# Kernel tuning notes

Measured on AMD Instinct MI355X. Metric: run time of the kernel, lower is better.

Reference implementation:

```python
import jax, jax.numpy as jnp
import numpy as np

B, LATENT, HID, OUT, E = 8192, 128, 400, 4096, 16

def setup_inputs() -> dict:
    key = jax.random.key(0)
    k = jax.random.split(key, 6)
    return {
        "z": jax.random.normal(k[0], (B, LATENT), dtype=jnp.float32),
        "W1": jax.random.normal(k[1], (E, HID, LATENT), dtype=jnp.float32) * (1.0 / np.sqrt(LATENT)),
        "b1": jax.random.normal(k[2], (E, HID), dtype=jnp.float32) * 0.01,
        "W2": jax.random.normal(k[3], (E, OUT, HID), dtype=jnp.float32) * (1.0 / np.sqrt(HID)),
        "b2": jax.random.normal(k[4], (E, OUT), dtype=jnp.float32) * 0.01,
        "angle_idx": jax.random.randint(k[5], (B,), 0, E, dtype=jnp.int64) if jax.config.jax_enable_x64 else jax.random.randint(k[5], (B,), 0, E, dtype=jnp.int32),
    }

def reference(z, W1, b1, W2, b2, angle_idx):
    # Per-sample expert select: out[i] = sigmoid(W2[e] @ relu(W1[e] @ z[i] + b1[e]) + b2[e]), e = angle_idx[i].
    # Dense-dispatch reference: run every expert on the full batch, select per-sample result.
    n_experts = W1.shape[0]
    out = jnp.zeros((z.shape[0], W2.shape[1]), dtype=z.dtype)
    for e in range(n_experts):  # small fixed loop over experts
        h = jax.nn.relu(z @ W1[e].T + b1[e])          # [B, 400]
        o = jax.nn.sigmoid(h @ W2[e].T + b2[e])       # [B, OUT]
        out = jnp.where((angle_idx == e)[:, None], o, out)
    return out
```

## Files before the change

### kernel.cpp

```cpp
#include <hip/hip_runtime.h>

#define BATCH  8192
#define LATENT 128
#define HID    400
#define HIDP   448
#define NOUT   4096
#define NE     16
#define HROWS  (BATCH + 256)

typedef __attribute__((ext_vector_type(8))) short bf16x8;
typedef __attribute__((ext_vector_type(4))) float f32x4;

__device__ __forceinline__ unsigned short f2bf(float f){
  unsigned u = __builtin_bit_cast(unsigned, f);
  u += 0x7fffu + ((u >> 16) & 1u);
  return (unsigned short)(u >> 16);
}

__device__ __forceinline__ void gload16(const void* g, void* l){
  __builtin_amdgcn_global_load_lds(
      (const __attribute__((address_space(1))) void*)g,
      (__attribute__((address_space(3))) void*)l, 16, 0, 0);
}

__global__ __launch_bounds__(1024) void k_prep(
    const int* __restrict__ aidx, int* __restrict__ wsI,
    const float* __restrict__ W2, unsigned short* __restrict__ W2b)
{
  int tid = threadIdx.x;
  if (blockIdx.x != 0){
    const int NSLOT = NE*NOUT*(HIDP/8);
    int g = ((int)blockIdx.x - 1)*1024 + tid;
    for (int i = g; i < NSLOT; i += 1536*1024){
      int row  = (int)((unsigned)i / 56u);
      int slot = i - row*56;
      int k = slot*8;
      bf16x8 w = (bf16x8){0,0,0,0,0,0,0,0};
      if (slot < 50){
        const float* s = W2 + (size_t)row*HID + k;
        f32x4 a = __builtin_nontemporal_load((const f32x4*)s);
        f32x4 b = __builtin_nontemporal_load((const f32x4*)(s+4));
        w[0]=(short)f2bf(a.x); w[1]=(short)f2bf(a.y); w[2]=(short)f2bf(a.z); w[3]=(short)f2bf(a.w);
        w[4]=(short)f2bf(b.x); w[5]=(short)f2bf(b.y); w[6]=(short)f2bf(b.z); w[7]=(short)f2bf(b.w);
      }
      __builtin_nontemporal_store(w, (bf16x8*)(W2b + (size_t)row*HIDP + k));
    }
    return;
  }
  __shared__ int hist[NE];
  __shared__ int cursor[NE];
  int lane = tid & 63;
  if (tid < NE) hist[tid] = 0;
  __syncthreads();

  int ev[8];
  #pragma unroll
  for (int c=0;c<8;c++) ev[c] = aidx[c*1024 + tid];

  #pragma unroll
  for (int c=0;c<8;c++){
    for (int x=0;x<NE;x++){
      unsigned long long m = __ballot(ev[c]==x);
      if (lane==0 && m) atomicAdd(&hist[x], (int)__popcll(m));
    }
  }
  __syncthreads();
  if (tid==0){
    int a=0;
    for (int x=0;x<NE;x++){ cursor[x]=a; wsI[32+x]=a; a+=hist[x]; }
    wsI[32+NE]=a;
  }
  __syncthreads();

  #pragma unroll
  for (int c=0;c<8;c++){
    int e = ev[c], i = c*1024 + tid;
    for (int x=0;x<NE;x++){
      unsigned long long m = __ballot(e==x);
      if (m){
        int leader = __ffsll((unsigned long long)m) - 1;
        int base = 0;
        if (lane == leader) base = atomicAdd(&cursor[x], (int)__popcll(m));
        base = __shfl(base, leader);
        if (e==x){
          int rank = (int)__popcll(m & ((1ull<<lane)-1ull));
          wsI[64 + base + rank] = i;
        }
      }
    }
  }
}

__global__ __launch_bounds__(256) void k_layer1(
    const float* __restrict__ z, const float* __restrict__ W1, const float* __restrict__ b1,
    const int* __restrict__ wsI, unsigned short* __restrict__ hws)
{
  __shared__ int s_off[NE+1];
  __shared__ int s_perm[64];
  __shared__ unsigned short As[64*128];
  __shared__ unsigned short Bs[64*128];
  int tid = threadIdx.x;
  if (tid <= NE) s_off[tid] = wsI[32+tid];
  __syncthreads();

  int e=-1, tile=0;
  { int acc=0;
    for (int i=0;i<NE;i++){
      int cnt = s_off[i+1]-s_off[i]; int t = (cnt+63)>>6;
      if ((int)blockIdx.x < acc+t){ e=i; tile=(int)blockIdx.x-acc; break; }
      acc += t; } }
  if (e < 0) return;
  int r0 = s_off[e] + tile*64;
  int rows = s_off[e+1] - r0; if (rows > 64) rows = 64;
  int n0 = blockIdx.y * 64;

  if (tid < 64) s_perm[tid] = (tid < rows) ? wsI[64 + r0 + tid] : 0;
  __syncthreads();

  #pragma unroll
  for (int p=0;p<8;p++){
    int id = tid + p*256; int row = id>>5, c4 = id&31;
    float4 v = make_float4(0.f,0.f,0.f,0.f);
    if (row < rows) v = *(const float4*)(z + (size_t)s_perm[row]*LATENT + c4*4);
    short4 w; w.x=(short)f2bf(v.x); w.y=(short)f2bf(v.y); w.z=(short)f2bf(v.z); w.w=(short)f2bf(v.w);
    *(short4*)((char*)As + row*256 + ((c4*8) ^ ((row&7)<<4))) = w;
  }
  const float* w1e = W1 + (size_t)e*HID*LATENT;
  #pragma unroll
  for (int p=0;p<8;p++){
    int id = tid + p*256; int row = id>>5, c4 = id&31;
    int n = n0 + row;
    float4 v = make_float4(0.f,0.f,0.f,0.f);
    if (n < HID) v = *(const float4*)(w1e + (size_t)n*LATENT + c4*4);
    short4 w; w.x=(short)f2bf(v.x); w.y=(short)f2bf(v.y); w.z=(short)f2bf(v.z); w.w=(short)f2bf(v.w);
    *(short4*)((char*)Bs + row*256 + ((c4*8) ^ ((row&7)<<4))) = w;
  }
  __syncthreads();

  int lane = tid & 63, wid = tid >> 6;
  int wm = wid >> 1, wn = wid & 1;
  int llo = lane & 15, lhi = lane >> 4;
  f32x4 acc[2][2];
  #pragma unroll
  for (int i=0;i<2;i++)
    #pragma unroll
    for (int j=0;j<2;j++) acc[i][j] = (f32x4){0.f,0.f,0.f,0.f};

  #pragma unroll
  for (int s=0;s<4;s++){
    bf16x8 af[2], bfr[2];
    #pragma unroll
    for (int i=0;i<2;i++){ int m = wm*32 + i*16 + llo;
      af[i] = *(bf16x8*)((char*)As + m*256 + ((s*64 + lhi*16) ^ ((m&7)<<4))); }
    #pragma unroll
    for (int j=0;j<2;j++){ int n = wn*32 + j*16 + llo;
      bfr[j] = *(bf16x8*)((char*)Bs + n*256 + ((s*64 + lhi*16) ^ ((n&7)<<4))); }
    #pragma unroll
    for (int i=0;i<2;i++)
      #pragma unroll
      for (int j=0;j<2;j++)
        acc[i][j] = __builtin_amdgcn_mfma_f32_16x16x32_bf16(af[i], bfr[j], acc[i][j], 0,0,0);
  }

  const float* b1e = b1 + e*HID;
  #pragma unroll
  for (int i=0;i<2;i++){
    #pragma unroll
    for (int j=0;j<2;j++){
      int n = n0 + wn*32 + j*16 + llo;
      float bias = (n < HID) ? b1e[n] : 0.f;
      #pragma unroll
      for (int q=0;q<4;q++){
        int m = wm*32 + i*16 + lhi*4 + q;
        if (m < rows){
          float v = acc[i][j][q] + bias;
          v = (v > 0.f) ? v : 0.f;
          if (n >= HID) v = 0.f;
          hws[(size_t)(r0+m)*HIDP + n] = f2bf(v);
        }
      }
    }
  }
}

__global__ __launch_bounds__(512) void k_layer2(
    const unsigned short* __restrict__ hws, const unsigned short* __restrict__ W2b,
    const float* __restrict__ b2, const int* __restrict__ wsI, float* __restrict__ out)
{
  __shared__ int s_off[NE+1];
  __shared__ int s_perm[256];
  __shared__ unsigned short As[256*64];
  __shared__ unsigned short Bs[128*64];
  int tid = threadIdx.x;
  if (tid <= NE) s_off[tid] = wsI[32+tid];
  __syncthreads();

  int lin = (int)blockIdx.x;
  int logical = (lin & 7) * 192 + (lin >> 3);
  int by = logical & 31;
  int bx = logical >> 5;

  int e=-1, tile=0;
  { int acc=0;
    for (int i=0;i<NE;i++){
      int cnt = s_off[i+1]-s_off[i]; int t = (cnt+255)>>8;
      if (bx < acc+t){ e=i; tile=bx-acc; break; }
      acc += t; } }
  if (e < 0) return;
  int r0 = s_off[e] + tile*256;
  int rows = s_off[e+1] - r0; if (rows > 256) rows = 256;
  int n0 = by * 128;
  if (tid < 256) s_perm[tid] = (tid < rows) ? wsI[64 + r0 + tid] : 0;

  int lane = tid & 63, w = tid >> 6;
  int srow = lane >> 3;
  int colU = (lane & 7) ^ srow;
  const unsigned short* aSrcBase = hws + (size_t)r0*HIDP + colU*8;
  const unsigned short* bSrcBase = W2b + ((size_t)e*NOUT + n0)*HIDP + colU*8;

  int wm = w >> 1, wn = w & 1;
  int llo = lane & 15, lhi = lane >> 4;
  f32x4 acc[4][4];
  #pragma unroll
  for (int i=0;i<4;i++)
    #pragma unroll
    for (int j=0;j<4;j++) acc[i][j] = (f32x4){0.f,0.f,0.f,0.f};

  #define STAGE(K0) { \
    _Pragma("unroll") for (int p=0;p<4;p++){ \
      int c = w*4 + p; int row = c*8 + srow; \
      gload16(aSrcBase + (size_t)row*HIDP + (K0), &As[c*512]); } \
    _Pragma("unroll") for (int p=0;p<2;p++){ \
      int c = w*2 + p; int row = c*8 + srow; \
      gload16(bSrcBase + (size_t)row*HIDP + (K0), &Bs[c*512]); } }

  for (int kt=0; kt<7; kt++){
    STAGE(kt*64);
    __syncthreads();
    #pragma unroll
    for (int s=0;s<2;s++){
      bf16x8 af[4], bfr[4];
      #pragma unroll
      for (int i=0;i<4;i++){ int m = wm*64 + i*16 + llo;
        af[i] = *(bf16x8*)((char*)As + m*128 + ((s*64 + lhi*16) ^ ((m&7)<<4))); }
      #pragma unroll
      for (int j=0;j<4;j++){ int n = wn*64 + j*16 + llo;
        bfr[j] = *(bf16x8*)((char*)Bs + n*128 + ((s*64 + lhi*16) ^ ((n&7)<<4))); }
      #pragma unroll
      for (int i=0;i<4;i++)
        #pragma unroll
        for (int j=0;j<4;j++)
          acc[i][j] = __builtin_amdgcn_mfma_f32_16x16x32_bf16(af[i], bfr[j], acc[i][j], 0,0,0);
    }
    __syncthreads();
  }

  const float* b2e = b2 + (size_t)e*NOUT;
  #pragma unroll
  for (int i=0;i<4;i++){
    int mb = wm*64 + i*16 + lhi*4;
    #pragma unroll
    for (int q=0;q<4;q++){
      int m = mb + q;
      if (m < rows){
        int orow = s_perm[m];
        float* op = out + (size_t)orow*NOUT + n0;
        #pragma unroll
        for (int j=0;j<4;j++){
          int nloc = wn*64 + j*16 + llo;
          float x = acc[i][j][q] + b2e[n0 + nloc];
          __builtin_nontemporal_store(1.f / (1.f + __expf(-x)), op + nloc);
        }
      }
    }
  }
}

extern "C" void kernel_launch(void* const* d_in, const int* in_sizes, int n_in,
                              void* d_out, int out_size, void* d_ws, size_t ws_size,
                              hipStream_t stream){
  const float* z   = (const float*)d_in[0];
  const float* W1  = (const float*)d_in[1];
  const float* b1  = (const float*)d_in[2];
  const float* W2  = (const float*)d_in[3];
  const float* b2  = (const float*)d_in[4];
  const int*  aidx = (const int*)d_in[5];
  float* out = (float*)d_out;
  int* wsI = (int*)d_ws;
  unsigned short* hws = (unsigned short*)((char*)d_ws + 65536);
  unsigned short* W2b = (unsigned short*)((char*)d_ws + 65536 + (size_t)HROWS*HIDP*2);

  k_prep  <<<1537, 1024, 0, stream>>>(aidx, wsI, W2, W2b);
  k_layer1<<<dim3(144, 7), 256, 0, stream>>>(z, W1, b1, wsI, hws);
  k_layer2<<<1536, 512, 0, stream>>>(hws, W2b, b2, wsI, out);
}
```

Before: 141.7 us.

## Move W2 bf16 conversion into layer-1 launch and split layer-1 K loop

Bucketing now runs alone in a single-block kernel. The W2 fp32-to-bf16 conversion moves into the layer-1 kernel as 2048 extra 256-thread blocks, so conversion and the layer-1 GEMM can run concurrently. Layer-1 tiles now load K in two 64-wide halves with half-size LDS buffers, which lowers shared memory per block and may allow more resident blocks, at the cost of an extra barrier. The layer-1 blocks now wait behind the conversion blocks in the same grid, and the single-block bucket kernel serialises ahead of everything else.

```diff
diff --git a/kernel.cpp b/kernel.cpp
--- a/kernel.cpp
+++ b/kernel.cpp
@@ -7,6 +7,7 @@
 #define NOUT   4096
 #define NE     16
 #define HROWS  (BATCH + 256)
+#define NCONV  2048
 
 typedef __attribute__((ext_vector_type(8))) short bf16x8;
 typedef __attribute__((ext_vector_type(4))) float f32x4;
@@ -23,33 +24,10 @@
       (__attribute__((address_space(3))) void*)l, 16, 0, 0);
 }
 
-__global__ __launch_bounds__(1024) void k_prep(
-    const int* __restrict__ aidx, int* __restrict__ wsI,
-    const float* __restrict__ W2, unsigned short* __restrict__ W2b)
-{
-  int tid = threadIdx.x;
-  if (blockIdx.x != 0){
-    const int NSLOT = NE*NOUT*(HIDP/8);
-    int g = ((int)blockIdx.x - 1)*1024 + tid;
-    for (int i = g; i < NSLOT; i += 1536*1024){
-      int row  = (int)((unsigned)i / 56u);
-      int slot = i - row*56;
-      int k = slot*8;
-      bf16x8 w = (bf16x8){0,0,0,0,0,0,0,0};
-      if (slot < 50){
-        const float* s = W2 + (size_t)row*HID + k;
-        f32x4 a = __builtin_nontemporal_load((const f32x4*)s);
-        f32x4 b = __builtin_nontemporal_load((const f32x4*)(s+4));
-        w[0]=(short)f2bf(a.x); w[1]=(short)f2bf(a.y); w[2]=(short)f2bf(a.z); w[3]=(short)f2bf(a.w);
-        w[4]=(short)f2bf(b.x); w[5]=(short)f2bf(b.y); w[6]=(short)f2bf(b.z); w[7]=(short)f2bf(b.w);
-      }
-      __builtin_nontemporal_store(w, (bf16x8*)(W2b + (size_t)row*HIDP + k));
-    }
-    return;
-  }
+__global__ __launch_bounds__(1024) void k_bucket(const int* __restrict__ aidx, int* __restrict__ wsI){
   __shared__ int hist[NE];
   __shared__ int cursor[NE];
-  int lane = tid & 63;
+  int tid = threadIdx.x, lane = tid & 63;
   if (tid < NE) hist[tid] = 0;
   __syncthreads();
 
@@ -91,55 +69,60 @@
   }
 }
 
-__global__ __launch_bounds__(256) void k_layer1(
+__global__ __launch_bounds__(256) void k_mid(
     const float* __restrict__ z, const float* __restrict__ W1, const float* __restrict__ b1,
-    const int* __restrict__ wsI, unsigned short* __restrict__ hws)
+    const int* __restrict__ wsI, unsigned short* __restrict__ hws,
+    const float* __restrict__ W2, unsigned short* __restrict__ W2b)
 {
+  int tid = threadIdx.x;
+  if (blockIdx.x < NCONV){
+    const int NSLOT = NE*NOUT*(HIDP/8);
+    int g = (int)blockIdx.x*256 + tid;
+    for (int i = g; i < NSLOT; i += NCONV*256){
+      int row  = (int)((unsigned)i / 56u);
+      int slot = i - row*56;
+      int k = slot*8;
+      bf16x8 w = (bf16x8){0,0,0,0,0,0,0,0};
+      if (slot < 50){
+        const float* s = W2 + (size_t)row*HID + k;
+        f32x4 a = __builtin_nontemporal_load((const f32x4*)s);
+        f32x4 b = __builtin_nontemporal_load((const f32x4*)(s+4));
+        w[0]=(short)f2bf(a.x); w[1]=(short)f2bf(a.y); w[2]=(short)f2bf(a.z); w[3]=(short)f2bf(a.w);
+        w[4]=(short)f2bf(b.x); w[5]=(short)f2bf(b.y); w[6]=(short)f2bf(b.z); w[7]=(short)f2bf(b.w);
+      }
+      __builtin_nontemporal_store(w, (bf16x8*)(W2b + (size_t)row*HIDP + k));
+    }
+    return;
+  }
+
   __shared__ int s_off[NE+1];
   __shared__ int s_perm[64];
-  __shared__ unsigned short As[64*128];
-  __shared__ unsigned short Bs[64*128];
-  int tid = threadIdx.x;
+  __shared__ unsigned short As[64*64];
+  __shared__ unsigned short Bs[64*64];
   if (tid <= NE) s_off[tid] = wsI[32+tid];
   __syncthreads();
+
+  int b2i = (int)blockIdx.x - NCONV;
+  int rt = b2i / 7;
+  int n0 = (b2i % 7) * 64;
 
   int e=-1, tile=0;
   { int acc=0;
     for (int i=0;i<NE;i++){
       int cnt = s_off[i+1]-s_off[i]; int t = (cnt+63)>>6;
-      if ((int)blockIdx.x < acc+t){ e=i; tile=(int)blockIdx.x-acc; break; }
+      if (rt < acc+t){ e=i; tile=rt-acc; break; }
       acc += t; } }
   if (e < 0) return;
   int r0 = s_off[e] + tile*64;
   int rows = s_off[e+1] - r0; if (rows > 64) rows = 64;
-  int n0 = blockIdx.y * 64;
 
   if (tid < 64) s_perm[tid] = (tid < rows) ? wsI[64 + r0 + tid] : 0;
-  __syncthreads();
-
-  #pragma unroll
-  for (int p=0;p<8;p++){
-    int id = tid + p*256; int row = id>>5, c4 = id&31;
-    float4 v = make_float4(0.f,0.f,0.f,0.f);
-    if (row < rows) v = *(const float4*)(z + (size_t)s_perm[row]*LATENT + c4*4);
-    short4 w; w.x=(short)f2bf(v.x); w.y=(short)f2bf(v.y); w.z=(short)f2bf(v.z); w.w=(short)f2bf(v.w);
-    *(short4*)((char*)As + row*256 + ((c4*8) ^ ((row&7)<<4))) = w;
-  }
-  const float* w1e = W1 + (size_t)e*HID*LATENT;
-  #pragma unroll
-  for (int p=0;p<8;p++){
-    int id = tid + p*256; int row = id>>5, c4 = id&31;
-    int n = n0 + row;
-    float4 v = make_float4(0.f,0.f,0.f,0.f);
-    if (n < HID) v = *(const float4*)(w1e + (size_t)n*LATENT + c4*4);
-    short4 w; w.x=(short)f2bf(v.x); w.y=(short)f2bf(v.y); w.z=(short)f2bf(v.z); w.w=(short)f2bf(v.w);
-    *(short4*)((char*)Bs + row*256 + ((c4*8) ^ ((row&7)<<4))) = w;
-  }
   __syncthreads();
 
   int lane = tid & 63, wid = tid >> 6;
   int wm = wid >> 1, wn = wid & 1;
   int llo = lane & 15, lhi = lane >> 4;
+  const float* w1e = W1 + (size_t)e*HID*LATENT;
   f32x4 acc[2][2];
   #pragma unroll
   for (int i=0;i<2;i++)
@@ -147,19 +130,41 @@
     for (int j=0;j<2;j++) acc[i][j] = (f32x4){0.f,0.f,0.f,0.f};
 
   #pragma unroll
-  for (int s=0;s<4;s++){
-    bf16x8 af[2], bfr[2];
-    #pragma unroll
-    for (int i=0;i<2;i++){ int m = wm*32 + i*16 + llo;
-      af[i] = *(bf16x8*)((char*)As + m*256 + ((s*64 + lhi*16) ^ ((m&7)<<4))); }
-    #pragma unroll
-    for (int j=0;j<2;j++){ int n = wn*32 + j*16 + llo;
-      bfr[j] = *(bf16x8*)((char*)Bs + n*256 + ((s*64 + lhi*16) ^ ((n&7)<<4))); }
-    #pragma unroll
-    for (int i=0;i<2;i++)
-      #pragma unroll
-      for (int j=0;j<2;j++)
-        acc[i][j] = __builtin_amdgcn_mfma_f32_16x16x32_bf16(af[i], bfr[j], acc[i][j], 0,0,0);
+  for (int kk=0; kk<2; kk++){
+    if (kk) __syncthreads();
+    #pragma unroll
+    for (int p=0;p<4;p++){
+      int id = tid + p*256; int row = id>>4, c4 = id&15;
+      float4 v = make_float4(0.f,0.f,0.f,0.f);
+      if (row < rows) v = *(const float4*)(z + (size_t)s_perm[row]*LATENT + kk*64 + c4*4);
+      short4 w; w.x=(short)f2bf(v.x); w.y=(short)f2bf(v.y); w.z=(short)f2bf(v.z); w.w=(short)f2bf(v.w);
+      *(short4*)((char*)As + row*128 + ((c4*8) ^ ((row&7)<<4))) = w;
+    }
+    #pragma unroll
+    for (int p=0;p<4;p++){
+      int id = tid + p*256; int row = id>>4, c4 = id&15;
+      int n = n0 + row;
+      float4 v = make_float4(0.f,0.f,0.f,0.f);
+      if (n < HID) v = *(const float4*)(w1e + (size_t)n*LATENT + kk*64 + c4*4);
+      short4 w; w.x=(short)f2bf(v.x); w.y=(short)f2bf(v.y); w.z=(short)f2bf(v.z); w.w=(short)f2bf(v.w);
+      *(short4*)((char*)Bs + row*128 + ((c4*8) ^ ((row&7)<<4))) = w;
+    }
+    __syncthreads();
+    #pragma unroll
+    for (int s=0;s<2;s++){
+      bf16x8 af[2], bfr[2];
+      #pragma unroll
+      for (int i=0;i<2;i++){ int m = wm*32 + i*16 + llo;
+        af[i] = *(bf16x8*)((char*)As + m*128 + ((s*64 + lhi*16) ^ ((m&7)<<4))); }
+      #pragma unroll
+      for (int j=0;j<2;j++){ int n = wn*32 + j*16 + llo;
+        bfr[j] = *(bf16x8*)((char*)Bs + n*128 + ((s*64 + lhi*16) ^ ((n&7)<<4))); }
+      #pragma unroll
+      for (int i=0;i<2;i++)
+        #pragma unroll
+        for (int j=0;j<2;j++)
+          acc[i][j] = __builtin_amdgcn_mfma_f32_16x16x32_bf16(af[i], bfr[j], acc[i][j], 0,0,0);
+    }
   }
 
   const float* b1e = b1 + e*HID;
@@ -290,7 +295,7 @@
   unsigned short* hws = (unsigned short*)((char*)d_ws + 65536);
   unsigned short* W2b = (unsigned short*)((char*)d_ws + 65536 + (size_t)HROWS*HIDP*2);
 
-  k_prep  <<<1537, 1024, 0, stream>>>(aidx, wsI, W2, W2b);
-  k_layer1<<<dim3(144, 7), 256, 0, stream>>>(z, W1, b1, wsI, hws);
+  k_bucket<<<1, 1024, 0, stream>>>(aidx, wsI);
+  k_mid   <<<NCONV + 1008, 256, 0, stream>>>(z, W1, b1, wsI, hws, W2, W2b);
   k_layer2<<<1536, 512, 0, stream>>>(hws, W2b, b2, wsI, out);
 }
```

Result: slower. 169.2 us (+19.4%).
